# Performance work log

Hardware: AMD Instinct MI355X
Metric: run time of the kernel (lower is better)

## Reference

```python
import jax, jax.numpy as jnp
import numpy as np

T, D, H, HD = 2048, 2048, 16, 128
ROPE_BASE = 10000.0
NEG = jnp.float32(-1e30)


def rms_norm(x):
    # F.rms_norm(x, (x.size(-1),)) with default eps = dtype eps
    eps = jnp.finfo(x.dtype).eps
    return x * jax.lax.rsqrt(jnp.mean(x * x, axis=-1, keepdims=True) + eps)


def rotary(x):
    # x: [1, T, H, hd]; half-split rotation as in Rotary.forward
    hd = x.shape[-1]
    inv_freq = (1.0 / ROPE_BASE) ** (jnp.arange(0, hd, 2, dtype=jnp.float32) / hd)
    t = jnp.arange(x.shape[1], dtype=jnp.float32)
    freqs = jnp.outer(t, inv_freq)                      # [T, hd/2]
    cos = jnp.cos(freqs)[None, :, None, :]
    sin = jnp.sin(freqs)[None, :, None, :]
    x1, x2 = jnp.split(x, 2, axis=-1)
    return jnp.concatenate([x1 * cos + x2 * sin, -x1 * sin + x2 * cos], axis=-1)


def setup_inputs() -> dict:
    key = jax.random.key(0)
    ks = jax.random.split(key, 10)
    w = lambda k, shape: jax.random.normal(k, shape, jnp.float32) * 0.02
    return {
        "x":  jax.random.normal(ks[0], (1, T, D), jnp.float32),
        "vi": jax.random.normal(ks[1], (1, T, H, HD), jnp.float32),
        "x0": jax.random.normal(ks[2], (1, T, D), jnp.float32),
        "wq": w(ks[3], (D, D)),
        "wk": w(ks[4], (D, D)),
        "wv": w(ks[5], (D, D)),
        "wo": w(ks[6], (D, D)),
        "lamb": jnp.float32(0.5),
        "lambdas": jnp.array([1.0, 0.0], jnp.float32),
        "w_fc": w(ks[7], (4 * D, D)),
        "w_proj": w(ks[8], (D, 4 * D)),
    }


def reference(x, vi, x0, wq, wk, wv, wo, lamb, lambdas, w_fc, w_proj):
    # Block: residual blend with initial embedding x0
    xb = lambdas[0] * x + lambdas[1] * x0
    xn = rms_norm(xb)

    # --- CausalSelfAttention ---
    q = (xn @ wq.T).reshape(1, T, H, HD)
    k = (xn @ wk.T).reshape(1, T, H, HD)
    v = (xn @ wv.T).reshape(1, T, H, HD)
    v = (1.0 - lamb) * v + lamb * vi                     # value-embedding blend
    q = rotary(rms_norm(q))
    k = rotary(rms_norm(k))

    scale = 1.0 / jnp.sqrt(jnp.float32(HD))              # flex_attention default scale
    scores = jnp.einsum('bqhd,bkhd->bhqk', q, k) * scale # [1,H,T,T]
    causal = jnp.tril(jnp.ones((T, T), bool))
    scores = jnp.where(causal[None, None], scores, NEG)
    attn = jax.nn.softmax(scores, axis=-1)
    y = jnp.einsum('bhqk,bkhd->bqhd', attn, v).reshape(1, T, D)
    a = y @ wo.T                                         # attention output REPLACES x (no residual)

    # --- MLP with squared ReLU ---
    h = rms_norm(a) @ w_fc.T
    h = jnp.square(jax.nn.relu(h))
    out = a + h @ w_proj.T
    return out
```

## Files before the change

### kernel.cpp

```cpp
#include <hip/hip_runtime.h>
#include <hip/hip_bf16.h>

typedef __bf16 bf16;
typedef __bf16 bf16x8 __attribute__((ext_vector_type(8)));
typedef float f32x4 __attribute__((ext_vector_type(4)));

#define DD 2048
#define DD2 4194304ull
#define G8_LDS 147456
#define G8_BUF 24576

__device__ __forceinline__ void glds16(const void* g, void* l) {
  __builtin_amdgcn_global_load_lds((const __attribute__((address_space(1))) void*)g,
                                   (__attribute__((address_space(3))) void*)l, 16, 0, 0);
}

__device__ __forceinline__ f32x4 mfma16(bf16x8 a, bf16x8 b, f32x4 c) {
  return __builtin_amdgcn_mfma_f32_16x16x32_bf16(a, b, c, 0, 0, 0);
}

__global__ __launch_bounds__(256) void cvt_bf16(const float* __restrict__ in, bf16* __restrict__ out) {
  size_t i = ((size_t)blockIdx.x * 256 + threadIdx.x) * 8;
  float4 a = *(const float4*)(in + i);
  float4 b = *(const float4*)(in + i + 4);
  bf16x8 o;
  o[0] = (bf16)a.x; o[1] = (bf16)a.y; o[2] = (bf16)a.z; o[3] = (bf16)a.w;
  o[4] = (bf16)b.x; o[5] = (bf16)b.y; o[6] = (bf16)b.z; o[7] = (bf16)b.w;
  *(bf16x8*)(out + i) = o;
}

template<bool BLEND>
__global__ __launch_bounds__(256) void prenorm_k(const float* __restrict__ x, const float* __restrict__ x0,
                                                 const float* __restrict__ lambdas, bf16* __restrict__ out) {
  const int t = blockIdx.x, tid = threadIdx.x;
  const float4* xr = (const float4*)(x + (size_t)t * DD);
  float4 a0 = xr[2 * tid], a1 = xr[2 * tid + 1];
  float v[8] = {a0.x, a0.y, a0.z, a0.w, a1.x, a1.y, a1.z, a1.w};
  if (BLEND) {
    const float l0 = lambdas[0], l1 = lambdas[1];
    const float4* yr = (const float4*)(x0 + (size_t)t * DD);
    float4 b0 = yr[2 * tid], b1 = yr[2 * tid + 1];
    float w[8] = {b0.x, b0.y, b0.z, b0.w, b1.x, b1.y, b1.z, b1.w};
#pragma unroll
    for (int i = 0; i < 8; ++i) v[i] = l0 * v[i] + l1 * w[i];
  }
  float ss = 0.f;
#pragma unroll
  for (int i = 0; i < 8; ++i) ss += v[i] * v[i];
#pragma unroll
  for (int off = 1; off < 64; off <<= 1) ss += __shfl_xor(ss, off, 64);
  __shared__ float red[4];
  const int wid = tid >> 6;
  if ((tid & 63) == 0) red[wid] = ss;
  __syncthreads();
  ss = red[0] + red[1] + red[2] + red[3];
  const float sc = rsqrtf(ss * (1.0f / DD) + 1.1920928955078125e-07f);
  bf16x8 o;
#pragma unroll
  for (int i = 0; i < 8; ++i) o[i] = (bf16)(v[i] * sc);
  *(bf16x8*)(out + (size_t)t * DD + tid * 8) = o;
}

__global__ __launch_bounds__(256) void rope_k(bf16* __restrict__ qg, bf16* __restrict__ kg) {
  const int tid = threadIdx.x, lane = tid & 63, wid = tid >> 6;
  const int p = blockIdx.x * 4 + wid;
  bf16* base = ((p >> 15) ? kg : qg);
  const int t = (p >> 4) & 2047, hh = p & 15;
  base += (size_t)t * DD + hh * 128;
  float x1 = (float)base[lane], x2 = (float)base[lane + 64];
  float ss = x1 * x1 + x2 * x2;
#pragma unroll
  for (int off = 1; off < 64; off <<= 1) ss += __shfl_xor(ss, off, 64);
  const float sc = rsqrtf(ss * (1.0f / 128.0f) + 1.1920928955078125e-07f);
  x1 *= sc; x2 *= sc;
  const float fr = (float)t * exp2f((float)lane * (-13.287712379549449f / 64.0f));
  const float s = sinf(fr), c = cosf(fr);
  base[lane]      = (bf16)(x1 * c + x2 * s);
  base[lane + 64] = (bf16)(-x1 * s + x2 * c);
}

__global__ __launch_bounds__(256) void vt_k(const bf16* __restrict__ v, bf16* __restrict__ vt) {
  __shared__ alignas(16) bf16 tile[16 * 128];
  const int tb = blockIdx.x, hb = blockIdx.y, tid = threadIdx.x;
  glds16(v + (size_t)(tb * 16 + (tid >> 4)) * DD + hb * 128 + (tid & 15) * 8, tile + tid * 8);
  __syncthreads();
  const int d_l = tid & 127, tc = tid >> 7;
  bf16x8 o;
#pragma unroll
  for (int i = 0; i < 8; ++i) o[i] = tile[(tc * 8 + i) * 128 + d_l];
  *(bf16x8*)(vt + (size_t)(hb * 128 + d_l) * DD + tb * 16 + tc * 8) = o;
}

__device__ __forceinline__ void g8_stageA(const bf16* A, int Kstride, int row0, int k0,
                                          bf16* buf, int tid, int i) {
  int e = tid + i * 256, row = e >> 3, slot = e & 7;
  glds16(A + (size_t)(row0 + row) * Kstride + k0 + ((slot ^ (row & 7)) * 8), buf + e * 8);
}
__device__ __forceinline__ void g8_stageB(const bf16* B, int Kstride, int col0, int k0,
                                          bf16* buf, int tid, int i) {
  int e = tid + i * 256, row = e >> 3, slot = e & 7;
  glds16(B + (size_t)(col0 + row) * Kstride + k0 + ((slot ^ (row & 7)) * 8), buf + 16384 + e * 8);
}

__device__ __forceinline__ void gemm8_core(const bf16* __restrict__ A, const bf16* __restrict__ B,
                                           int Kstride, int Klen, int row0, int col0,
                                           bf16* smem, f32x4 (&acc)[8][4]) {
  const int tid = threadIdx.x, lane = tid & 63, wid = tid >> 6;
  const int wm = wid >> 1, wn = wid & 1;
  const int l15 = lane & 15, g = lane >> 4;
  const int NT = Klen >> 6;
#pragma unroll
  for (int i = 0; i < 8; ++i) g8_stageA(A, Kstride, row0, 0, smem, tid, i);
#pragma unroll
  for (int i = 0; i < 4; ++i) g8_stageB(B, Kstride, col0, 0, smem, tid, i);
#pragma unroll
  for (int i = 0; i < 8; ++i) g8_stageA(A, Kstride, row0, 64, smem + G8_BUF, tid, i);
#pragma unroll
  for (int i = 0; i < 4; ++i) g8_stageB(B, Kstride, col0, 64, smem + G8_BUF, tid, i);
  asm volatile("s_waitcnt vmcnt(12)" ::: "memory");
  __builtin_amdgcn_s_barrier();

  int cur = 0, sb = 2;
  for (int t = 0; t < NT; ++t) {
    bf16* Ab = smem + cur * G8_BUF;
    bf16* Bb = Ab + 16384;
    bf16* Sb = smem + sb * G8_BUF;
    const int ks0 = (t + 2) * 64;
    const bool st = (t + 2) < NT;
    bf16x8 a[4][2], b0[2][2], b1[2][2];
#pragma unroll
    for (int mm = 0; mm < 4; ++mm)
#pragma unroll
      for (int ks = 0; ks < 2; ++ks) {
        int row = wm * 128 + mm * 16 + l15;
        a[mm][ks] = *(const bf16x8*)(Ab + row * 64 + (((ks * 4 + g) ^ (row & 7)) * 8));
      }
#pragma unroll
    for (int nn = 0; nn < 2; ++nn)
#pragma unroll
      for (int ks = 0; ks < 2; ++ks) {
        int row = wn * 64 + nn * 16 + l15;
        b0[nn][ks] = *(const bf16x8*)(Bb + row * 64 + (((ks * 4 + g) ^ (row & 7)) * 8));
      }
    if (st) { g8_stageA(A, Kstride, row0, ks0, Sb, tid, 0);
              g8_stageA(A, Kstride, row0, ks0, Sb, tid, 1);
              g8_stageA(A, Kstride, row0, ks0, Sb, tid, 2); }
    __builtin_amdgcn_s_setprio(1);
#pragma unroll
    for (int mm = 0; mm < 4; ++mm)
#pragma unroll
      for (int nn = 0; nn < 2; ++nn)
#pragma unroll
        for (int ks = 0; ks < 2; ++ks)
          acc[mm][nn] = mfma16(a[mm][ks], b0[nn][ks], acc[mm][nn]);
    __builtin_amdgcn_s_setprio(0);
    __builtin_amdgcn_s_barrier();
#pragma unroll
    for (int nn = 0; nn < 2; ++nn)
#pragma unroll
      for (int ks = 0; ks < 2; ++ks) {
        int row = wn * 64 + 32 + nn * 16 + l15;
        b1[nn][ks] = *(const bf16x8*)(Bb + row * 64 + (((ks * 4 + g) ^ (row & 7)) * 8));
      }
    if (st) { g8_stageA(A, Kstride, row0, ks0, Sb, tid, 3);
              g8_stageA(A, Kstride, row0, ks0, Sb, tid, 4);
              g8_stageA(A, Kstride, row0, ks0, Sb, tid, 5); }
    __builtin_amdgcn_s_setprio(1);
#pragma unroll
    for (int mm = 0; mm < 4; ++mm)
#pragma unroll
      for (int nn = 0; nn < 2; ++nn)
#pragma unroll
        for (int ks = 0; ks < 2; ++ks)
          acc[mm][2 + nn] = mfma16(a[mm][ks], b1[nn][ks], acc[mm][2 + nn]);
    __builtin_amdgcn_s_setprio(0);
    __builtin_amdgcn_s_barrier();
#pragma unroll
    for (int mm = 0; mm < 4; ++mm)
#pragma unroll
      for (int ks = 0; ks < 2; ++ks) {
        int row = wm * 128 + 64 + mm * 16 + l15;
        a[mm][ks] = *(const bf16x8*)(Ab + row * 64 + (((ks * 4 + g) ^ (row & 7)) * 8));
      }
    if (st) { g8_stageA(A, Kstride, row0, ks0, Sb, tid, 6);
              g8_stageA(A, Kstride, row0, ks0, Sb, tid, 7);
              g8_stageB(B, Kstride, col0, ks0, Sb, tid, 0); }
    __builtin_amdgcn_s_setprio(1);
#pragma unroll
    for (int mm = 0; mm < 4; ++mm)
#pragma unroll
      for (int nn = 0; nn < 2; ++nn)
#pragma unroll
        for (int ks = 0; ks < 2; ++ks)
          acc[4 + mm][nn] = mfma16(a[mm][ks], b0[nn][ks], acc[4 + mm][nn]);
    __builtin_amdgcn_s_setprio(0);
    __builtin_amdgcn_s_barrier();
    if (st) { g8_stageB(B, Kstride, col0, ks0, Sb, tid, 1);
              g8_stageB(B, Kstride, col0, ks0, Sb, tid, 2);
              g8_stageB(B, Kstride, col0, ks0, Sb, tid, 3); }
    __builtin_amdgcn_s_setprio(1);
#pragma unroll
    for (int mm = 0; mm < 4; ++mm)
#pragma unroll
      for (int nn = 0; nn < 2; ++nn)
#pragma unroll
        for (int ks = 0; ks < 2; ++ks)
          acc[4 + mm][2 + nn] = mfma16(a[mm][ks], b1[nn][ks], acc[4 + mm][2 + nn]);
    __builtin_amdgcn_s_setprio(0);
    if (st) { asm volatile("s_waitcnt vmcnt(12)" ::: "memory"); }
    else if (t + 1 < NT) { asm volatile("s_waitcnt vmcnt(0)" ::: "memory"); }
    __builtin_amdgcn_s_barrier();
    cur = (cur == 2) ? 0 : cur + 1;
    sb = (sb == 2) ? 0 : sb + 1;
  }
}

#define GEMM8_EPI(STMT)                                                       \
  { const int lane_ = threadIdx.x & 63, wid_ = threadIdx.x >> 6;              \
    const int l15_ = lane_ & 15, g_ = lane_ >> 4;                             \
    const int wr_ = (wid_ >> 1) * 128, wc_ = (wid_ & 1) * 64;                 \
    _Pragma("unroll") for (int m = 0; m < 8; ++m)                             \
    _Pragma("unroll") for (int n = 0; n < 4; ++n)                             \
    _Pragma("unroll") for (int j = 0; j < 4; ++j) {                           \
      int grow = row0 + wr_ + m * 16 + g_ * 4 + j;                            \
      int gcol = col0 + wc_ + n * 16 + l15_;                                  \
      float vacc = acc[m][n][j];                                              \
      STMT; } }

__global__ __launch_bounds__(256, 1) void gemm8_qkv(const bf16* __restrict__ A,
    const bf16* __restrict__ Wq, const bf16* __restrict__ Wk, const bf16* __restrict__ Wv,
    bf16* __restrict__ oq, bf16* __restrict__ ok, bf16* __restrict__ ov,
    const float* __restrict__ vi, const float* __restrict__ lambp) {
  extern __shared__ bf16 smem8[];
  const int z = blockIdx.z;
  const bf16* B = (z == 0) ? Wq : (z == 1) ? Wk : Wv;
  bf16* out = (z == 0) ? oq : (z == 1) ? ok : ov;
  const int row0 = blockIdx.y * 256, col0 = blockIdx.x * 128;
  f32x4 acc[8][4] = {};
  gemm8_core(A, B, DD, DD, row0, col0, smem8, acc);
  if (z < 2) {
    GEMM8_EPI( out[(size_t)grow * DD + gcol] = (bf16)vacc; )
  } else {
    const float lam = *lambp;
    GEMM8_EPI( out[(size_t)grow * DD + gcol] =
                 (bf16)((1.0f - lam) * vacc + lam * vi[(size_t)grow * DD + gcol]); )
  }
}

template<int EPI>
__global__ __launch_bounds__(256, 1) void gemm8_ep(const bf16* __restrict__ A, const bf16* __restrict__ B,
                                                   void* __restrict__ outv, int N, int Kstride, int Klen) {
  extern __shared__ bf16 smem8[];
  const int row0 = blockIdx.y * 256, col0 = blockIdx.x * 128;
  const int kofs = blockIdx.z * Klen;
  f32x4 acc[8][4] = {};
  gemm8_core(A + kofs, B + kofs, Kstride, Klen, row0, col0, smem8, acc);
  if (EPI == 2) { float* out = (float*)outv + (size_t)blockIdx.z * DD2;
    GEMM8_EPI( out[(size_t)grow * N + gcol] = vacc; ) }
  if (EPI == 3) { bf16* out = (bf16*)outv;
    GEMM8_EPI( float r = fmaxf(vacc, 0.f); out[(size_t)grow * N + gcol] = (bf16)(r * r); ) }
}

__global__ __launch_bounds__(256) void wo_red_prenorm(const float* __restrict__ p, float* __restrict__ a_f,
                                                      bf16* __restrict__ an) {
  const int t = blockIdx.x, tid = threadIdx.x;
  const size_t base = (size_t)t * DD + tid * 8;
  float4 a0 = *(const float4*)(p + base),        a1 = *(const float4*)(p + base + 4);
  float4 b0 = *(const float4*)(p + DD2 + base),  b1 = *(const float4*)(p + DD2 + base + 4);
  float v[8] = {a0.x + b0.x, a0.y + b0.y, a0.z + b0.z, a0.w + b0.w,
                a1.x + b1.x, a1.y + b1.y, a1.z + b1.z, a1.w + b1.w};
  *(float4*)(a_f + base)     = make_float4(v[0], v[1], v[2], v[3]);
  *(float4*)(a_f + base + 4) = make_float4(v[4], v[5], v[6], v[7]);
  float ss = 0.f;
#pragma unroll
  for (int i = 0; i < 8; ++i) ss += v[i] * v[i];
#pragma unroll
  for (int off = 1; off < 64; off <<= 1) ss += __shfl_xor(ss, off, 64);
  __shared__ float red[4];
  if ((tid & 63) == 0) red[tid >> 6] = ss;
  __syncthreads();
  ss = red[0] + red[1] + red[2] + red[3];
  const float sc = rsqrtf(ss * (1.0f / DD) + 1.1920928955078125e-07f);
  bf16x8 o;
#pragma unroll
  for (int i = 0; i < 8; ++i) o[i] = (bf16)(v[i] * sc);
  *(bf16x8*)(an + base) = o;
}

__global__ __launch_bounds__(256) void proj_red(const float* __restrict__ p, const float* __restrict__ a_f,
                                                float* __restrict__ out) {
  const size_t base = ((size_t)blockIdx.x * 256 + threadIdx.x) * 8;
#pragma unroll
  for (int h = 0; h < 2; ++h) {
    size_t i = base + h * 4;
    float4 r = *(const float4*)(a_f + i);
    float4 u = *(const float4*)(p + i);
    float4 w = *(const float4*)(p + DD2 + i);
    *(float4*)(out + i) = make_float4(r.x + u.x + w.x, r.y + u.y + w.y,
                                      r.z + u.z + w.z, r.w + u.w + w.w);
  }
}

__global__ __launch_bounds__(256) void attn_k(const bf16* __restrict__ qg, const bf16* __restrict__ kg,
                                              const bf16* __restrict__ vtg, bf16* __restrict__ yg) {
  __shared__ alignas(16) bf16 Ks[32 * 128];
  __shared__ alignas(16) bf16 Vt[128 * 32];
  __shared__ alignas(16) bf16 Pl[4][16 * 32];
  const int h = blockIdx.y, qb = 31 - blockIdx.x;
  const int tid = threadIdx.x, lane = tid & 63, wid = tid >> 6;
  const int l15 = lane & 15, g = lane >> 4;
  const int qrow = qb * 64 + wid * 16;
  const float scale = 0.08838834764831845f;
  bf16x8 aQ[4];
  {
    const bf16* qp = qg + (size_t)(qrow + l15) * DD + h * 128 + g * 8;
#pragma unroll
    for (int kc = 0; kc < 4; ++kc) aQ[kc] = *(const bf16x8*)(qp + kc * 32);
  }
  f32x4 acc[8] = {};
  f32x4 l4 = {0.f, 0.f, 0.f, 0.f};
  const int nkt = qb * 2 + 2;
  for (int kt = 0; kt < nkt; ++kt) {
    const int kbase = kt * 32;
    __syncthreads();
#pragma unroll
    for (int r = 0; r < 2; ++r) {
      int e = tid + r * 256;
      int row = e >> 4, slot = e & 15;
      glds16(kg + (size_t)(kbase + row) * DD + h * 128 + ((slot ^ (row & 7)) * 8), Ks + e * 8);
    }
#pragma unroll
    for (int r = 0; r < 2; ++r) {
      int e = tid + r * 256;
      int d = e >> 2, slot = e & 3;
      glds16(vtg + (size_t)(h * 128 + d) * DD + kbase + ((slot ^ (d & 3)) * 8), Vt + e * 8);
    }
    __syncthreads();
    f32x4 S0 = {}, S1 = {};
#pragma unroll
    for (int kc = 0; kc < 4; ++kc) {
      int r0 = l15, r1 = 16 + l15;
      bf16x8 b0 = *(const bf16x8*)(Ks + r0 * 128 + (((kc * 4 + g) ^ (r0 & 7)) * 8));
      bf16x8 b1 = *(const bf16x8*)(Ks + r1 * 128 + (((kc * 4 + g) ^ (r1 & 7)) * 8));
      S0 = mfma16(aQ[kc], b0, S0);
      S1 = mfma16(aQ[kc], b1, S1);
    }
    const int k0i = kbase + l15, k1i = k0i + 16;
    f32x4 p0, p1;
#pragma unroll
    for (int j = 0; j < 4; ++j) {
      int q = qrow + g * 4 + j;
      p0[j] = (k0i <= q) ? __expf(S0[j] * scale) : 0.f;
      p1[j] = (k1i <= q) ? __expf(S1[j] * scale) : 0.f;
      l4[j] += p0[j] + p1[j];
    }
    const int c0 = (l15 >> 3) ^ g, c1 = (2 + (l15 >> 3)) ^ g, w7 = l15 & 7;
#pragma unroll
    for (int j = 0; j < 4; ++j) {
      Pl[wid][(g * 4 + j) * 32 + c0 * 8 + w7] = (bf16)p0[j];
      Pl[wid][(g * 4 + j) * 32 + c1 * 8 + w7] = (bf16)p1[j];
    }
    bf16x8 aP = *(const bf16x8*)(&Pl[wid][l15 * 32 + ((g ^ (l15 >> 2)) * 8)]);
#pragma unroll
    for (int dt = 0; dt < 8; ++dt) {
      int d = dt * 16 + l15;
      bf16x8 bV = *(const bf16x8*)(Vt + d * 32 + ((g ^ (d & 3)) * 8));
      acc[dt] = mfma16(aP, bV, acc[dt]);
    }
  }
#pragma unroll
  for (int off = 1; off < 16; off <<= 1)
#pragma unroll
    for (int j = 0; j < 4; ++j) l4[j] += __shfl_xor(l4[j], off, 64);
#pragma unroll
  for (int dt = 0; dt < 8; ++dt)
#pragma unroll
    for (int j = 0; j < 4; ++j) {
      int q = qrow + g * 4 + j;
      yg[(size_t)q * DD + h * 128 + dt * 16 + l15] = (bf16)(acc[dt][j] / l4[j]);
    }
}

extern "C" void kernel_launch(void* const* d_in, const int* in_sizes, int n_in,
                              void* d_out, int out_size, void* d_ws, size_t ws_size,
                              hipStream_t stream) {
  const float* x       = (const float*)d_in[0];
  const float* vi      = (const float*)d_in[1];
  const float* x0      = (const float*)d_in[2];
  const float* wq      = (const float*)d_in[3];
  const float* wk      = (const float*)d_in[4];
  const float* wv      = (const float*)d_in[5];
  const float* wo      = (const float*)d_in[6];
  const float* lamb    = (const float*)d_in[7];
  const float* lambdas = (const float*)d_in[8];
  const float* wfc     = (const float*)d_in[9];
  const float* wproj   = (const float*)d_in[10];
  float* out = (float*)d_out;

  (void)hipFuncSetAttribute(reinterpret_cast<const void*>(gemm8_qkv),
                            hipFuncAttributeMaxDynamicSharedMemorySize, G8_LDS);
  (void)hipFuncSetAttribute(reinterpret_cast<const void*>(gemm8_ep<2>),
                            hipFuncAttributeMaxDynamicSharedMemorySize, G8_LDS);
  (void)hipFuncSetAttribute(reinterpret_cast<const void*>(gemm8_ep<3>),
                            hipFuncAttributeMaxDynamicSharedMemorySize, G8_LDS);

  char* wsb = (char*)d_ws;
  size_t off = 0;
  auto alloc = [&](size_t bytes) { void* p = wsb + off; off = (off + bytes + 255) & ~(size_t)255; return p; };
  bf16* wq_b  = (bf16*)alloc(DD2 * 2);
  bf16* wk_b  = (bf16*)alloc(DD2 * 2);
  bf16* wv_b  = (bf16*)alloc(DD2 * 2);
  bf16* wo_b  = (bf16*)alloc(DD2 * 2);
  bf16* wfc_b = (bf16*)alloc(DD2 * 8);
  bf16* wpj_b = (bf16*)alloc(DD2 * 8);
  bf16* xn_b  = (bf16*)alloc(DD2 * 2);
  bf16* q_b   = (bf16*)alloc(DD2 * 2);
  bf16* k_b   = (bf16*)alloc(DD2 * 2);
  bf16* v_b   = (bf16*)alloc(DD2 * 2);
  float* part = (float*)xn_b;
  bf16* y_b   = (bf16*)alloc(DD2 * 2);
  float* a_f  = (float*)alloc(DD2 * 4);
  bf16* an_b  = (bf16*)alloc(DD2 * 2);
  bf16* h_b   = (bf16*)alloc(DD2 * 8);
  bf16* vt_b  = h_b;

  cvt_bf16<<<2048, 256, 0, stream>>>(wq, wq_b);
  cvt_bf16<<<2048, 256, 0, stream>>>(wk, wk_b);
  cvt_bf16<<<2048, 256, 0, stream>>>(wv, wv_b);
  cvt_bf16<<<2048, 256, 0, stream>>>(wo, wo_b);
  cvt_bf16<<<8192, 256, 0, stream>>>(wfc, wfc_b);
  cvt_bf16<<<8192, 256, 0, stream>>>(wproj, wpj_b);

  prenorm_k<true><<<2048, 256, 0, stream>>>(x, x0, lambdas, xn_b);
  gemm8_qkv<<<dim3(16, 8, 3), 256, G8_LDS, stream>>>(xn_b, wq_b, wk_b, wv_b, q_b, k_b, v_b, vi, lamb);
  rope_k<<<16384, 256, 0, stream>>>(q_b, k_b);
  vt_k<<<dim3(128, 16), 256, 0, stream>>>(v_b, vt_b);
  attn_k<<<dim3(32, 16), 256, 0, stream>>>(q_b, k_b, vt_b, y_b);
  gemm8_ep<2><<<dim3(16, 8, 2), 256, G8_LDS, stream>>>(y_b, wo_b, (void*)part, DD, DD, 1024);
  wo_red_prenorm<<<2048, 256, 0, stream>>>(part, a_f, an_b);
  gemm8_ep<3><<<dim3(64, 8, 1), 256, G8_LDS, stream>>>(an_b, wfc_b, (void*)h_b, 4 * DD, DD, DD);
  gemm8_ep<2><<<dim3(16, 8, 2), 256, G8_LDS, stream>>>(h_b, wpj_b, (void*)part, DD, 4 * DD, 4096);
  proj_red<<<2048, 256, 0, stream>>>(part, a_f, out);
}
```

Measured before the change: 440.4 us.

## Switch GEMMs to 256x256 tiles with 8 waves and double buffering

Replaces the 256x128 4-wave triple-buffered GEMM core with a 256x256 tile computed by 512 threads (8 waves), double-buffered in 128KB LDS with staged half-tile loads and finer waitcnt/barrier sync. The proj GEMM split-K becomes a 3-way split of uneven length (2752) to fill more CUs, with the final reduction reading three partials. The six weight-conversion launches are merged into one kernel. Larger tiles raise data reuse per LDS byte, but the change also cuts the block count, uses two-deep instead of three-deep prefetch, and adds barriers.

```diff
diff --git a/kernel.cpp b/kernel.cpp
--- a/kernel.cpp
+++ b/kernel.cpp
@@ -7,8 +7,7 @@
 
 #define DD 2048
 #define DD2 4194304ull
-#define G8_LDS 147456
-#define G8_BUF 24576
+#define G9_LDS 131072
 
 __device__ __forceinline__ void glds16(const void* g, void* l) {
   __builtin_amdgcn_global_load_lds((const __attribute__((address_space(1))) void*)g,
@@ -19,14 +18,23 @@
   return __builtin_amdgcn_mfma_f32_16x16x32_bf16(a, b, c, 0, 0, 0);
 }
 
-__global__ __launch_bounds__(256) void cvt_bf16(const float* __restrict__ in, bf16* __restrict__ out) {
-  size_t i = ((size_t)blockIdx.x * 256 + threadIdx.x) * 8;
-  float4 a = *(const float4*)(in + i);
-  float4 b = *(const float4*)(in + i + 4);
+__global__ __launch_bounds__(256) void cvt_all(const float* __restrict__ s0, const float* __restrict__ s1,
+                                               const float* __restrict__ s2, const float* __restrict__ s3,
+                                               const float* __restrict__ s4, const float* __restrict__ s5,
+                                               bf16* __restrict__ dbase) {
+  const int b = blockIdx.x;
+  const float* src; bf16* dst; int lb;
+  if (b < 8192)       { int r = b >> 11; src = (r == 0) ? s0 : (r == 1) ? s1 : (r == 2) ? s2 : s3;
+                        dst = dbase + (size_t)r * DD2; lb = b & 2047; }
+  else if (b < 16384) { src = s4; dst = dbase + 4 * DD2; lb = b - 8192; }
+  else                { src = s5; dst = dbase + 8 * DD2; lb = b - 16384; }
+  size_t i = ((size_t)lb * 256 + threadIdx.x) * 8;
+  float4 a = *(const float4*)(src + i);
+  float4 c = *(const float4*)(src + i + 4);
   bf16x8 o;
   o[0] = (bf16)a.x; o[1] = (bf16)a.y; o[2] = (bf16)a.z; o[3] = (bf16)a.w;
-  o[4] = (bf16)b.x; o[5] = (bf16)b.y; o[6] = (bf16)b.z; o[7] = (bf16)b.w;
-  *(bf16x8*)(out + i) = o;
+  o[4] = (bf16)c.x; o[5] = (bf16)c.y; o[6] = (bf16)c.z; o[7] = (bf16)c.w;
+  *(bf16x8*)(dst + i) = o;
 }
 
 template<bool BLEND>
@@ -91,60 +99,65 @@
   *(bf16x8*)(vt + (size_t)(hb * 128 + d_l) * DD + tb * 16 + tc * 8) = o;
 }
 
-__device__ __forceinline__ void g8_stageA(const bf16* A, int Kstride, int row0, int k0,
-                                          bf16* buf, int tid, int i) {
-  int e = tid + i * 256, row = e >> 3, slot = e & 7;
-  glds16(A + (size_t)(row0 + row) * Kstride + k0 + ((slot ^ (row & 7)) * 8), buf + e * 8);
-}
-__device__ __forceinline__ void g8_stageB(const bf16* B, int Kstride, int col0, int k0,
-                                          bf16* buf, int tid, int i) {
-  int e = tid + i * 256, row = e >> 3, slot = e & 7;
-  glds16(B + (size_t)(col0 + row) * Kstride + k0 + ((slot ^ (row & 7)) * 8), buf + 16384 + e * 8);
-}
-
-__device__ __forceinline__ void gemm8_core(const bf16* __restrict__ A, const bf16* __restrict__ B,
+__device__ __forceinline__ void g9_stageA(const bf16* A, int Kstride, int row0, int k0,
+                                          bf16* buf, int hm, int tid) {
+#pragma unroll
+  for (int i = 0; i < 2; ++i) {
+    int e = tid + i * 512;
+    int prl = e >> 3, slot = e & 7;
+    int wm = prl >> 6, r63 = prl & 63;
+    glds16(A + (size_t)(row0 + wm * 128 + hm * 64 + r63) * Kstride + k0 + ((slot ^ (prl & 7)) * 8),
+           buf + hm * 8192 + e * 8);
+  }
+}
+__device__ __forceinline__ void g9_stageB(const bf16* B, int Kstride, int col0, int k0,
+                                          bf16* buf, int hn, int tid) {
+#pragma unroll
+  for (int i = 0; i < 2; ++i) {
+    int e = tid + i * 512;
+    int pbl = e >> 3, slot = e & 7;
+    int wn = pbl >> 5, q = pbl & 31;
+    glds16(B + (size_t)(col0 + wn * 64 + hn * 32 + q) * Kstride + k0 + ((slot ^ (pbl & 7)) * 8),
+           buf + 16384 + hn * 8192 + e * 8);
+  }
+}
+
+__device__ __forceinline__ void gemm9_core(const bf16* __restrict__ A, const bf16* __restrict__ B,
                                            int Kstride, int Klen, int row0, int col0,
                                            bf16* smem, f32x4 (&acc)[8][4]) {
   const int tid = threadIdx.x, lane = tid & 63, wid = tid >> 6;
-  const int wm = wid >> 1, wn = wid & 1;
+  const int wm = wid >> 2, wn = wid & 3;
   const int l15 = lane & 15, g = lane >> 4;
+  const int sw = l15 & 7;
   const int NT = Klen >> 6;
-#pragma unroll
-  for (int i = 0; i < 8; ++i) g8_stageA(A, Kstride, row0, 0, smem, tid, i);
-#pragma unroll
-  for (int i = 0; i < 4; ++i) g8_stageB(B, Kstride, col0, 0, smem, tid, i);
-#pragma unroll
-  for (int i = 0; i < 8; ++i) g8_stageA(A, Kstride, row0, 64, smem + G8_BUF, tid, i);
-#pragma unroll
-  for (int i = 0; i < 4; ++i) g8_stageB(B, Kstride, col0, 64, smem + G8_BUF, tid, i);
-  asm volatile("s_waitcnt vmcnt(12)" ::: "memory");
-  __builtin_amdgcn_s_barrier();
-
-  int cur = 0, sb = 2;
+  g9_stageA(A, Kstride, row0, 0, smem, 0, tid);
+  g9_stageB(B, Kstride, col0, 0, smem, 0, tid);
+  g9_stageB(B, Kstride, col0, 0, smem, 1, tid);
+  g9_stageA(A, Kstride, row0, 0, smem, 1, tid);
+
+  bf16x8 a[4][2], b0[2][2], b1[2][2];
   for (int t = 0; t < NT; ++t) {
-    bf16* Ab = smem + cur * G8_BUF;
-    bf16* Bb = Ab + 16384;
-    bf16* Sb = smem + sb * G8_BUF;
-    const int ks0 = (t + 2) * 64;
-    const bool st = (t + 2) < NT;
-    bf16x8 a[4][2], b0[2][2], b1[2][2];
+    bf16* cb = smem + (t & 1) * 32768;
+    bf16* sb = smem + ((t + 1) & 1) * 32768;
+    const int ks0 = (t + 1) << 6;
+    const bool st = (t + 1) < NT;
+    asm volatile("s_waitcnt vmcnt(4)" ::: "memory");
+    __builtin_amdgcn_s_barrier();
 #pragma unroll
     for (int mm = 0; mm < 4; ++mm)
 #pragma unroll
       for (int ks = 0; ks < 2; ++ks) {
-        int row = wm * 128 + mm * 16 + l15;
-        a[mm][ks] = *(const bf16x8*)(Ab + row * 64 + (((ks * 4 + g) ^ (row & 7)) * 8));
+        int pr = wm * 64 + mm * 16 + l15;
+        a[mm][ks] = *(const bf16x8*)(cb + pr * 64 + (((ks * 4 + g) ^ sw) * 8));
       }
 #pragma unroll
     for (int nn = 0; nn < 2; ++nn)
 #pragma unroll
       for (int ks = 0; ks < 2; ++ks) {
-        int row = wn * 64 + nn * 16 + l15;
-        b0[nn][ks] = *(const bf16x8*)(Bb + row * 64 + (((ks * 4 + g) ^ (row & 7)) * 8));
+        int pb = wn * 32 + nn * 16 + l15;
+        b0[nn][ks] = *(const bf16x8*)(cb + 16384 + pb * 64 + (((ks * 4 + g) ^ sw) * 8));
       }
-    if (st) { g8_stageA(A, Kstride, row0, ks0, Sb, tid, 0);
-              g8_stageA(A, Kstride, row0, ks0, Sb, tid, 1);
-              g8_stageA(A, Kstride, row0, ks0, Sb, tid, 2); }
+    if (st) g9_stageA(A, Kstride, row0, ks0, sb, 0, tid);
     __builtin_amdgcn_s_setprio(1);
 #pragma unroll
     for (int mm = 0; mm < 4; ++mm)
@@ -155,16 +168,17 @@
           acc[mm][nn] = mfma16(a[mm][ks], b0[nn][ks], acc[mm][nn]);
     __builtin_amdgcn_s_setprio(0);
     __builtin_amdgcn_s_barrier();
+    if (st) { asm volatile("s_waitcnt vmcnt(4)" ::: "memory"); }
+    else    { asm volatile("s_waitcnt vmcnt(2)" ::: "memory"); }
+    __builtin_amdgcn_s_barrier();
 #pragma unroll
     for (int nn = 0; nn < 2; ++nn)
 #pragma unroll
       for (int ks = 0; ks < 2; ++ks) {
-        int row = wn * 64 + 32 + nn * 16 + l15;
-        b1[nn][ks] = *(const bf16x8*)(Bb + row * 64 + (((ks * 4 + g) ^ (row & 7)) * 8));
+        int pb = 128 + wn * 32 + nn * 16 + l15;
+        b1[nn][ks] = *(const bf16x8*)(cb + 16384 + pb * 64 + (((ks * 4 + g) ^ sw) * 8));
       }
-    if (st) { g8_stageA(A, Kstride, row0, ks0, Sb, tid, 3);
-              g8_stageA(A, Kstride, row0, ks0, Sb, tid, 4);
-              g8_stageA(A, Kstride, row0, ks0, Sb, tid, 5); }
+    if (st) g9_stageB(B, Kstride, col0, ks0, sb, 0, tid);
     __builtin_amdgcn_s_setprio(1);
 #pragma unroll
     for (int mm = 0; mm < 4; ++mm)
@@ -175,16 +189,17 @@
           acc[mm][2 + nn] = mfma16(a[mm][ks], b1[nn][ks], acc[mm][2 + nn]);
     __builtin_amdgcn_s_setprio(0);
     __builtin_amdgcn_s_barrier();
+    if (st) { asm volatile("s_waitcnt vmcnt(4)" ::: "memory"); }
+    else    { asm volatile("s_waitcnt vmcnt(0)" ::: "memory"); }
+    __builtin_amdgcn_s_barrier();
 #pragma unroll
     for (int mm = 0; mm < 4; ++mm)
 #pragma unroll
       for (int ks = 0; ks < 2; ++ks) {
-        int row = wm * 128 + 64 + mm * 16 + l15;
-        a[mm][ks] = *(const bf16x8*)(Ab + row * 64 + (((ks * 4 + g) ^ (row & 7)) * 8));
+        int pr = 128 + wm * 64 + mm * 16 + l15;
+        a[mm][ks] = *(const bf16x8*)(cb + pr * 64 + (((ks * 4 + g) ^ sw) * 8));
       }
-    if (st) { g8_stageA(A, Kstride, row0, ks0, Sb, tid, 6);
-              g8_stageA(A, Kstride, row0, ks0, Sb, tid, 7);
-              g8_stageB(B, Kstride, col0, ks0, Sb, tid, 0); }
+    if (st) g9_stageB(B, Kstride, col0, ks0, sb, 1, tid);
     __builtin_amdgcn_s_setprio(1);
 #pragma unroll
     for (int mm = 0; mm < 4; ++mm)
@@ -195,9 +210,7 @@
           acc[4 + mm][nn] = mfma16(a[mm][ks], b0[nn][ks], acc[4 + mm][nn]);
     __builtin_amdgcn_s_setprio(0);
     __builtin_amdgcn_s_barrier();
-    if (st) { g8_stageB(B, Kstride, col0, ks0, Sb, tid, 1);
-              g8_stageB(B, Kstride, col0, ks0, Sb, tid, 2);
-              g8_stageB(B, Kstride, col0, ks0, Sb, tid, 3); }
+    if (st) g9_stageA(A, Kstride, row0, ks0, sb, 1, tid);
     __builtin_amdgcn_s_setprio(1);
 #pragma unroll
     for (int mm = 0; mm < 4; ++mm)
@@ -207,58 +220,56 @@
         for (int ks = 0; ks < 2; ++ks)
           acc[4 + mm][2 + nn] = mfma16(a[mm][ks], b1[nn][ks], acc[4 + mm][2 + nn]);
     __builtin_amdgcn_s_setprio(0);
-    if (st) { asm volatile("s_waitcnt vmcnt(12)" ::: "memory"); }
-    else if (t + 1 < NT) { asm volatile("s_waitcnt vmcnt(0)" ::: "memory"); }
-    __builtin_amdgcn_s_barrier();
-    cur = (cur == 2) ? 0 : cur + 1;
-    sb = (sb == 2) ? 0 : sb + 1;
-  }
-}
-
-#define GEMM8_EPI(STMT)                                                       \
-  { const int lane_ = threadIdx.x & 63, wid_ = threadIdx.x >> 6;              \
-    const int l15_ = lane_ & 15, g_ = lane_ >> 4;                             \
-    const int wr_ = (wid_ >> 1) * 128, wc_ = (wid_ & 1) * 64;                 \
-    _Pragma("unroll") for (int m = 0; m < 8; ++m)                             \
-    _Pragma("unroll") for (int n = 0; n < 4; ++n)                             \
-    _Pragma("unroll") for (int j = 0; j < 4; ++j) {                           \
-      int grow = row0 + wr_ + m * 16 + g_ * 4 + j;                            \
-      int gcol = col0 + wc_ + n * 16 + l15_;                                  \
-      float vacc = acc[m][n][j];                                              \
+    __builtin_amdgcn_s_barrier();
+  }
+}
+
+#define GEMM9_EPI(STMT)                                                        \
+  { const int lane_ = threadIdx.x & 63, wid_ = threadIdx.x >> 6;               \
+    const int l15_ = lane_ & 15, g_ = lane_ >> 4;                              \
+    const int wm_ = wid_ >> 2, wn_ = wid_ & 3;                                 \
+    _Pragma("unroll") for (int m = 0; m < 8; ++m)                              \
+    _Pragma("unroll") for (int n = 0; n < 4; ++n)                              \
+    _Pragma("unroll") for (int j = 0; j < 4; ++j) {                            \
+      int grow = row0 + wm_ * 128 + (m >> 2) * 64 + (m & 3) * 16 + g_ * 4 + j; \
+      int gcol = col0 + wn_ * 64 + (n >> 1) * 32 + (n & 1) * 16 + l15_;        \
+      float vacc = acc[m][n][j];                                               \
       STMT; } }
 
-__global__ __launch_bounds__(256, 1) void gemm8_qkv(const bf16* __restrict__ A,
+__global__ __launch_bounds__(512, 1) void gemm9_qkv(const bf16* __restrict__ A,
     const bf16* __restrict__ Wq, const bf16* __restrict__ Wk, const bf16* __restrict__ Wv,
     bf16* __restrict__ oq, bf16* __restrict__ ok, bf16* __restrict__ ov,
     const float* __restrict__ vi, const float* __restrict__ lambp) {
-  extern __shared__ bf16 smem8[];
+  extern __shared__ bf16 smem9[];
   const int z = blockIdx.z;
   const bf16* B = (z == 0) ? Wq : (z == 1) ? Wk : Wv;
   bf16* out = (z == 0) ? oq : (z == 1) ? ok : ov;
-  const int row0 = blockIdx.y * 256, col0 = blockIdx.x * 128;
+  const int row0 = blockIdx.y * 256, col0 = blockIdx.x * 256;
   f32x4 acc[8][4] = {};
-  gemm8_core(A, B, DD, DD, row0, col0, smem8, acc);
+  gemm9_core(A, B, DD, DD, row0, col0, smem9, acc);
   if (z < 2) {
-    GEMM8_EPI( out[(size_t)grow * DD + gcol] = (bf16)vacc; )
+    GEMM9_EPI( out[(size_t)grow * DD + gcol] = (bf16)vacc; )
   } else {
     const float lam = *lambp;
-    GEMM8_EPI( out[(size_t)grow * DD + gcol] =
+    GEMM9_EPI( out[(size_t)grow * DD + gcol] =
                  (bf16)((1.0f - lam) * vacc + lam * vi[(size_t)grow * DD + gcol]); )
   }
 }
 
 template<int EPI>
-__global__ __launch_bounds__(256, 1) void gemm8_ep(const bf16* __restrict__ A, const bf16* __restrict__ B,
-                                                   void* __restrict__ outv, int N, int Kstride, int Klen) {
-  extern __shared__ bf16 smem8[];
-  const int row0 = blockIdx.y * 256, col0 = blockIdx.x * 128;
-  const int kofs = blockIdx.z * Klen;
+__global__ __launch_bounds__(512, 1) void gemm9_ep(const bf16* __restrict__ A, const bf16* __restrict__ B,
+                                                   void* __restrict__ outv, int N, int Kstride,
+                                                   int KlenMain, int Ktot) {
+  extern __shared__ bf16 smem9[];
+  const int row0 = blockIdx.y * 256, col0 = blockIdx.x * 256;
+  const int kofs = blockIdx.z * KlenMain;
+  const int Klen = min(KlenMain, Ktot - kofs);
   f32x4 acc[8][4] = {};
-  gemm8_core(A + kofs, B + kofs, Kstride, Klen, row0, col0, smem8, acc);
+  gemm9_core(A + kofs, B + kofs, Kstride, Klen, row0, col0, smem9, acc);
   if (EPI == 2) { float* out = (float*)outv + (size_t)blockIdx.z * DD2;
-    GEMM8_EPI( out[(size_t)grow * N + gcol] = vacc; ) }
+    GEMM9_EPI( out[(size_t)grow * N + gcol] = vacc; ) }
   if (EPI == 3) { bf16* out = (bf16*)outv;
-    GEMM8_EPI( float r = fmaxf(vacc, 0.f); out[(size_t)grow * N + gcol] = (bf16)(r * r); ) }
+    GEMM9_EPI( float r = fmaxf(vacc, 0.f); out[(size_t)grow * N + gcol] = (bf16)(r * r); ) }
 }
 
 __global__ __launch_bounds__(256) void wo_red_prenorm(const float* __restrict__ p, float* __restrict__ a_f,
@@ -296,8 +307,9 @@
     float4 r = *(const float4*)(a_f + i);
     float4 u = *(const float4*)(p + i);
     float4 w = *(const float4*)(p + DD2 + i);
-    *(float4*)(out + i) = make_float4(r.x + u.x + w.x, r.y + u.y + w.y,
-                                      r.z + u.z + w.z, r.w + u.w + w.w);
+    float4 z = *(const float4*)(p + 2 * DD2 + i);
+    *(float4*)(out + i) = make_float4(r.x + u.x + w.x + z.x, r.y + u.y + w.y + z.y,
+                                      r.z + u.z + w.z + z.z, r.w + u.w + w.w + z.w);
   }
 }
 
@@ -397,12 +409,12 @@
   const float* wproj   = (const float*)d_in[10];
   float* out = (float*)d_out;
 
-  (void)hipFuncSetAttribute(reinterpret_cast<const void*>(gemm8_qkv),
-                            hipFuncAttributeMaxDynamicSharedMemorySize, G8_LDS);
-  (void)hipFuncSetAttribute(reinterpret_cast<const void*>(gemm8_ep<2>),
-                            hipFuncAttributeMaxDynamicSharedMemorySize, G8_LDS);
-  (void)hipFuncSetAttribute(reinterpret_cast<const void*>(gemm8_ep<3>),
-                            hipFuncAttributeMaxDynamicSharedMemorySize, G8_LDS);
+  (void)hipFuncSetAttribute(reinterpret_cast<const void*>(gemm9_qkv),
+                            hipFuncAttributeMaxDynamicSharedMemorySize, G9_LDS);
+  (void)hipFuncSetAttribute(reinterpret_cast<const void*>(gemm9_ep<2>),
+                            hipFuncAttributeMaxDynamicSharedMemorySize, G9_LDS);
+  (void)hipFuncSetAttribute(reinterpret_cast<const void*>(gemm9_ep<3>),
+                            hipFuncAttributeMaxDynamicSharedMemorySize, G9_LDS);
 
   char* wsb = (char*)d_ws;
   size_t off = 0;
@@ -417,28 +429,22 @@
   bf16* q_b   = (bf16*)alloc(DD2 * 2);
   bf16* k_b   = (bf16*)alloc(DD2 * 2);
   bf16* v_b   = (bf16*)alloc(DD2 * 2);
+  bf16* y_b   = (bf16*)alloc(DD2 * 2);
+  bf16* an_b  = (bf16*)alloc(DD2 * 2);
   float* part = (float*)xn_b;
-  bf16* y_b   = (bf16*)alloc(DD2 * 2);
   float* a_f  = (float*)alloc(DD2 * 4);
-  bf16* an_b  = (bf16*)alloc(DD2 * 2);
   bf16* h_b   = (bf16*)alloc(DD2 * 8);
   bf16* vt_b  = h_b;
 
-  cvt_bf16<<<2048, 256, 0, stream>>>(wq, wq_b);
-  cvt_bf16<<<2048, 256, 0, stream>>>(wk, wk_b);
-  cvt_bf16<<<2048, 256, 0, stream>>>(wv, wv_b);
-  cvt_bf16<<<2048, 256, 0, stream>>>(wo, wo_b);
-  cvt_bf16<<<8192, 256, 0, stream>>>(wfc, wfc_b);
-  cvt_bf16<<<8192, 256, 0, stream>>>(wproj, wpj_b);
-
+  cvt_all<<<24576, 256, 0, stream>>>(wq, wk, wv, wo, wfc, wproj, (bf16*)wsb);
   prenorm_k<true><<<2048, 256, 0, stream>>>(x, x0, lambdas, xn_b);
-  gemm8_qkv<<<dim3(16, 8, 3), 256, G8_LDS, stream>>>(xn_b, wq_b, wk_b, wv_b, q_b, k_b, v_b, vi, lamb);
+  gemm9_qkv<<<dim3(8, 8, 3), 512, G9_LDS, stream>>>(xn_b, wq_b, wk_b, wv_b, q_b, k_b, v_b, vi, lamb);
   rope_k<<<16384, 256, 0, stream>>>(q_b, k_b);
   vt_k<<<dim3(128, 16), 256, 0, stream>>>(v_b, vt_b);
   attn_k<<<dim3(32, 16), 256, 0, stream>>>(q_b, k_b, vt_b, y_b);
-  gemm8_ep<2><<<dim3(16, 8, 2), 256, G8_LDS, stream>>>(y_b, wo_b, (void*)part, DD, DD, 1024);
+  gemm9_ep<2><<<dim3(8, 8, 2), 512, G9_LDS, stream>>>(y_b, wo_b, (void*)part, DD, DD, 1024, DD);
   wo_red_prenorm<<<2048, 256, 0, stream>>>(part, a_f, an_b);
-  gemm8_ep<3><<<dim3(64, 8, 1), 256, G8_LDS, stream>>>(an_b, wfc_b, (void*)h_b, 4 * DD, DD, DD);
-  gemm8_ep<2><<<dim3(16, 8, 2), 256, G8_LDS, stream>>>(h_b, wpj_b, (void*)part, DD, 4 * DD, 4096);
+  gemm9_ep<3><<<dim3(32, 8, 1), 512, G9_LDS, stream>>>(an_b, wfc_b, (void*)h_b, 4 * DD, DD, DD, DD);
+  gemm9_ep<2><<<dim3(8, 8, 3), 512, G9_LDS, stream>>>(h_b, wpj_b, (void*)part, DD, 4 * DD, 2752, 4 * DD);
   proj_red<<<2048, 256, 0, stream>>>(part, a_f, out);
 }
```

New measurement: 407.2 us. 1.08x faster.
